# Optimization experiments

Hardware: AMD Instinct MI355X
Metric: run time of the kernel (lower is better)

Reference implementation:

```python
import jax, jax.numpy as jnp
import numpy as np

N_VERTS = 2562


def _uniform(key, shape, bound):
    return jax.random.uniform(key, shape, jnp.float32, -bound, bound)


def vert_align(feat, pos):
    # feat: [B,C,H,W]; pos: [B,N,3], xy in [-1,1] -> bilinear sample -> [B,N,C]
    B, C, H, W = feat.shape
    ft = jnp.transpose(feat, (0, 2, 3, 1))  # [B,H,W,C]
    x = (jnp.clip(pos[..., 0], -1.0, 1.0) + 1.0) * 0.5 * (W - 1)
    y = (jnp.clip(pos[..., 1], -1.0, 1.0) + 1.0) * 0.5 * (H - 1)
    x0 = jnp.floor(x)
    y0 = jnp.floor(y)
    x0i = x0.astype(jnp.int32)
    y0i = y0.astype(jnp.int32)
    x1i = jnp.minimum(x0i + 1, W - 1)
    y1i = jnp.minimum(y0i + 1, H - 1)
    wx = (x - x0)[..., None]
    wy = (y - y0)[..., None]
    b = jnp.arange(B)[:, None]
    f00 = ft[b, y0i, x0i]
    f01 = ft[b, y0i, x1i]
    f10 = ft[b, y1i, x0i]
    f11 = ft[b, y1i, x1i]
    return (f00 * (1 - wx) * (1 - wy) + f01 * wx * (1 - wy)
            + f10 * (1 - wx) * wy + f11 * wx * wy)


def graph_conv(x, adj, w0, w1):
    # relu(x @ w0 + adj @ (x @ w1))
    return jax.nn.relu(x @ w0 + jnp.einsum('bij,bjc->bic', adj, x @ w1))


def setup_inputs() -> dict:
    key = jax.random.key(0)
    ks = jax.random.split(key, 20)
    B, N = 8, N_VERTS
    inp = {
        'conv2_3': jax.random.normal(ks[0], (B, 256, 56, 56), jnp.float32),
        'conv3_4': jax.random.normal(ks[1], (B, 512, 28, 28), jnp.float32),
        'conv4_6': jax.random.normal(ks[2], (B, 1024, 14, 14), jnp.float32),
        'conv5_3': jax.random.normal(ks[3], (B, 2048, 7, 7), jnp.float32),
        # scaled so row sums are O(1), like a normalized dense adjacency
        'vertex_adjacency': jax.random.uniform(ks[4], (B, N, N), jnp.float32) * (2.0 / N),
        'vertex_positions': jax.random.uniform(ks[5], (B, N, 3), jnp.float32) * 2.0 - 1.0,
        'vertex_features': jax.random.normal(ks[6], (B, N, 128), jnp.float32),
    }
    # learned parameters (torch default / GraphConv uniform init)
    inp['w_lin0'] = _uniform(ks[7], (3840, 128), 1.0 / np.sqrt(3840))
    inp['b_lin0'] = _uniform(ks[8], (128,), 1.0 / np.sqrt(3840))
    inp['gc0_w0'] = _uniform(ks[9], (259, 131), 1.0 / np.sqrt(259))
    inp['gc0_w1'] = _uniform(ks[10], (259, 131), 1.0 / np.sqrt(259))
    inp['gc1_w0'] = _uniform(ks[11], (131, 128), 1.0 / np.sqrt(131))
    inp['gc1_w1'] = _uniform(ks[12], (131, 128), 1.0 / np.sqrt(131))
    inp['gc2_w0'] = _uniform(ks[13], (131, 128), 1.0 / np.sqrt(131))
    inp['gc2_w1'] = _uniform(ks[14], (131, 128), 1.0 / np.sqrt(131))
    inp['w_lin1'] = _uniform(ks[15], (128, 3), 1.0 / np.sqrt(128))
    inp['b_lin1'] = _uniform(ks[16], (3,), 1.0 / np.sqrt(128))
    return inp


def reference(conv2_3, conv3_4, conv4_6, conv5_3, vertex_adjacency,
              vertex_positions, vertex_features,
              w_lin0, b_lin0, gc0_w0, gc0_w1, gc1_w0, gc1_w1,
              gc2_w0, gc2_w1, w_lin1, b_lin1):
    verts = jnp.concatenate(
        [vert_align(f, vertex_positions)
         for f in (conv2_3, conv3_4, conv4_6, conv5_3)], axis=2)  # [B,N,3840]
    projected = verts @ w_lin0 + b_lin0                             # [B,N,128]
    vf = jnp.concatenate([vertex_features, vertex_positions, projected], axis=2)  # 259
    h = graph_conv(vf, vertex_adjacency, gc0_w0, gc0_w1)            # [B,N,131]
    h = jnp.concatenate([vertex_positions, h], axis=2)              # 134? no: 3+131=134 -- see note
    h = graph_conv(h[:, :, :131] if h.shape[2] != 131 else h, vertex_adjacency, gc1_w0, gc1_w1)
    h = jnp.concatenate([vertex_positions, h], axis=2)              # 131
    new_features = graph_conv(h, vertex_adjacency, gc2_w0, gc2_w1)  # [B,N,128]
    new_positions = vertex_positions + jnp.tanh(new_features @ w_lin1 + b_lin1)
    return new_positions, new_features
```

## Files before the change

kernel.cpp:

```cpp
#include <hip/hip_runtime.h>
#include <hip/hip_bf16.h>

typedef __attribute__((ext_vector_type(8))) short bf16x8;
typedef __attribute__((ext_vector_type(4))) float f32x4;
typedef __attribute__((ext_vector_type(2))) float f32x2;

static __device__ __forceinline__ float bf2f(unsigned short u){
  return __uint_as_float(((unsigned)u) << 16);
}
static __device__ __forceinline__ float bflo(unsigned v){ return __uint_as_float(v << 16); }
static __device__ __forceinline__ float bfhi(unsigned v){ return __uint_as_float(v & 0xffff0000u); }
static __device__ __forceinline__ unsigned short f2bf(float f){
  unsigned u = __float_as_uint(f);
  u += 0x7FFFu + ((u >> 16) & 1u);
  return (unsigned short)(u >> 16);
}
static __device__ __forceinline__ void gload_lds16(const void* g, void* l){
  __builtin_amdgcn_global_load_lds((const __attribute__((address_space(1))) unsigned int*)g,
                                   (__attribute__((address_space(3))) unsigned int*)l, 16, 0, 0);
}

#define MFMA16(acc, a, b) (acc) = __builtin_amdgcn_mfma_f32_16x16x32_bf16((a),(b),(acc),0,0,0)

#define NB   8
#define NVRT 2562
#define MP   2624
#define NRB2 82
#define NKT  41

#define FT_B0 0ul
#define FT_B1 6422528ul
#define FT_B2 9633792ul
#define FT_B3 11239424ul
#define FT_TOT 12042240ul

#define G_B0 0ul
#define G_B1 3211264ul
#define G_B2 4014080ul
#define G_B3 4214784ul
#define G_TOT 4264960ul

__global__ void k_transpose_all(const float* __restrict__ c0, const float* __restrict__ c1,
                                const float* __restrict__ c2, const float* __restrict__ c3,
                                unsigned short* __restrict__ ftT)
{
  __shared__ float tile[32][33];
  int bx = blockIdx.x, b = blockIdx.y;
  int m, local;
  if (bx < 784)      { m = 0; local = bx; }
  else if (bx < 1184){ m = 1; local = bx - 784; }
  else if (bx < 1408){ m = 2; local = bx - 1184; }
  else               { m = 3; local = bx - 1408; }
  int HW  = (m==0)?3136:(m==1)?784:(m==2)?196:49;
  int C   = 256 << m;
  int nbx = (m==0)?98:(m==1)?25:(m==2)?7:2;
  size_t fb = (m==0)?FT_B0:(m==1)?FT_B1:(m==2)?FT_B2:FT_B3;
  const float* src = (m==0)?c0:(m==1)?c1:(m==2)?c2:c3;

  int hw0 = (local % nbx) * 32, c0i = (local / nbx) * 32;
  int tx = threadIdx.x, ty = threadIdx.y;
  const float* s = src + (size_t)b * C * HW;
#pragma unroll
  for (int i = 0; i < 4; i++){
    int c = c0i + ty + i*8, hw = hw0 + tx;
    tile[ty + i*8][tx] = (c < C && hw < HW) ? s[(size_t)c * HW + hw] : 0.f;
  }
  __syncthreads();
  unsigned short* d = ftT + fb + (size_t)b * HW * C;
#pragma unroll
  for (int i = 0; i < 4; i++){
    int hw = hw0 + ty + i*8, c = c0i + tx;
    if (hw < HW && c < C) d[(size_t)hw * C + c] = f2bf(tile[tx][ty + i*8]);
  }
}

struct PWArgs {
  const float* src[7];
  unsigned short* dst[7];
  int ksrc[7], nsrc[7];
};
__global__ void k_packw_all(PWArgs a)
{
  const int cb[8] = {0,491520,528384,565248,585728,606208,626688,647168};
  int g = blockIdx.x * 256 + threadIdx.x;
#pragma unroll
  for (int s = 0; s < 7; s++){
    if (g >= cb[s] && g < cb[s+1]){
      int li = g - cb[s];
      int k = li >> 7, c = li & 127;
      int ks = a.ksrc[s], ns = a.nsrc[s];
      float v = (k < ks) ? a.src[s][(size_t)k * ns + c] : 0.f;
      a.dst[s][((size_t)(k >> 3) * 128 + c) * 8 + (k & 7)] = f2bf(v);
    }
  }
}

__global__ __launch_bounds__(256) void k_gproj(
    const unsigned short* __restrict__ ftT,
    const unsigned short* __restrict__ wp,
    unsigned short* __restrict__ G)
{
  int bx = blockIdx.x;
  int m, tile;
  if (bx < 784)      { m = 0; tile = bx; }
  else if (bx < 980) { m = 1; tile = bx - 784; }
  else if (bx < 1029){ m = 2; tile = bx - 980; }
  else               { m = 3; tile = bx - 1029; }
  int C    = 256 << m;
  int rows = 8 * ((m==0)?3136:(m==1)?784:(m==2)?196:49);
  size_t fb = (m==0)?FT_B0:(m==1)?FT_B1:(m==2)?FT_B2:FT_B3;
  size_t gb = (m==0)?G_B0:(m==1)?G_B1:(m==2)?G_B2:G_B3;
  int ko8 = ((m==0)?0:(m==1)?256:(m==2)?768:1792) >> 3;

  int t = threadIdx.x, wave = t >> 6, lane = t & 63;
  int rf = wave & 1, ch = wave >> 1;
  int l15 = lane & 15, l4 = lane >> 4;
  int row = tile*32 + rf*16 + l15;
  int arow = (row < rows) ? row : 0;
  const unsigned short* xp = ftT + fb + (size_t)arow * C + l4 * 8;

  f32x4 acc[4];
#pragma unroll
  for (int c = 0; c < 4; c++) acc[c] = (f32x4){0,0,0,0};

  for (int kb = 0; kb < C; kb += 32){
    bf16x8 a = *(const bf16x8*)(xp + kb);
    size_t bo = ((size_t)(ko8 + (kb>>3) + l4) * 128 + ch*64 + l15) * 8;
#pragma unroll
    for (int c = 0; c < 4; c++){
      bf16x8 bb = *(const bf16x8*)(wp + bo + c*128);
      MFMA16(acc[c], a, bb);
    }
  }
#pragma unroll
  for (int c = 0; c < 4; c++){
    int col = ch*64 + c*16 + l15;
#pragma unroll
    for (int r = 0; r < 4; r++){
      int orow = tile*32 + rf*16 + l4*4 + r;
      if (orow < rows) G[gb + (size_t)orow*128 + col] = f2bf(acc[c][r]);
    }
  }
}

__global__ void k_prep2(const float* __restrict__ vfeat, const float* __restrict__ pos,
                        const unsigned short* __restrict__ G,
                        const float* __restrict__ bias,
                        unsigned short* __restrict__ vf,
                        unsigned short* __restrict__ x1,
                        unsigned short* __restrict__ x2)
{
  int b = blockIdx.y;
  int row = blockIdx.x * 4 + (threadIdx.x >> 6);
  int lane = threadIdx.x & 63;
  size_t vfo = ((size_t)b * MP + row) * 288;
  size_t xo  = ((size_t)b * MP + row) * 160;
  if (row < NVRT){
    size_t src = (size_t)b * NVRT + row;
    float px = fminf(fmaxf(pos[src*3 + 0], -1.f), 1.f);
    float py = fminf(fmaxf(pos[src*3 + 1], -1.f), 1.f);
    int c0 = lane * 2;
    float s0 = bias[c0], s1 = bias[c0 + 1];
#pragma unroll
    for (int m = 0; m < 4; m++){
      int W = 56 >> m;
      int HW = W * W;
      size_t gb = (m==0)?G_B0:(m==1)?G_B1:(m==2)?G_B2:G_B3;
      float gx = (px + 1.f) * 0.5f * (float)(W - 1);
      float gy = (py + 1.f) * 0.5f * (float)(W - 1);
      int x0 = (int)floorf(gx), y0 = (int)floorf(gy);
      float wx = gx - (float)x0, wy = gy - (float)y0;
      int x1i = min(x0 + 1, W - 1), y1i = min(y0 + 1, W - 1);
      const unsigned short* g = G + gb + (size_t)b * HW * 128;
      unsigned v00 = *(const unsigned*)(g + ((size_t)(y0 *W + x0 ))*128 + c0);
      unsigned v01 = *(const unsigned*)(g + ((size_t)(y0 *W + x1i))*128 + c0);
      unsigned v10 = *(const unsigned*)(g + ((size_t)(y1i*W + x0 ))*128 + c0);
      unsigned v11 = *(const unsigned*)(g + ((size_t)(y1i*W + x1i))*128 + c0);
      float w00 = (1.f-wx)*(1.f-wy), w01 = wx*(1.f-wy);
      float w10 = (1.f-wx)*wy,       w11 = wx*wy;
      s0 += w00*bflo(v00) + w01*bflo(v01) + w10*bflo(v10) + w11*bflo(v11);
      s1 += w00*bfhi(v00) + w01*bfhi(v01) + w10*bfhi(v10) + w11*bfhi(v11);
    }
    vf[vfo + 131 + c0]     = f2bf(s0);
    vf[vfo + 131 + c0 + 1] = f2bf(s1);
    float2 fv = *(const float2*)(vfeat + src*128 + c0);
    vf[vfo + c0]     = f2bf(fv.x);
    vf[vfo + c0 + 1] = f2bf(fv.y);
    if (lane < 3){
      unsigned short v = f2bf(pos[src*3 + lane]);
      vf[vfo + 128 + lane] = v;
      x1[xo + lane] = v;
      x2[xo + lane] = v;
    }
    if (lane >= 32 && lane < 61) vf[vfo + 259 + (lane - 32)] = 0;
    if (lane < 29){ x1[xo + 131 + lane] = 0; x2[xo + 131 + lane] = 0; }
  } else {
    for (int c = lane; c < 288; c += 64) vf[vfo + c] = 0;
    for (int c = lane; c < 160; c += 64){ x1[xo + c] = 0; x2[xo + c] = 0; }
  }
}

__global__ void k_adjpack(const float* __restrict__ adj, unsigned short* __restrict__ adjP)
{
  int kt = blockIdx.x, rb = blockIdx.y, b = blockIdx.z;
  int t = threadIdx.x, row = t >> 3, k8 = t & 7;
  int grow = rb*32 + row, gk = kt*64 + k8*8;
  unsigned short o[8];
  if (grow < NVRT && gk + 8 <= NVRT){
    const float2* p = (const float2*)(adj + ((size_t)b*NVRT + grow)*NVRT + gk);
    float2 f0 = p[0], f1 = p[1], f2 = p[2], f3 = p[3];
    o[0]=f2bf(f0.x); o[1]=f2bf(f0.y); o[2]=f2bf(f1.x); o[3]=f2bf(f1.y);
    o[4]=f2bf(f2.x); o[5]=f2bf(f2.y); o[6]=f2bf(f3.x); o[7]=f2bf(f3.y);
  } else if (grow < NVRT){
    const float* ap = adj + ((size_t)b*NVRT + grow)*NVRT;
#pragma unroll
    for (int e = 0; e < 8; e++){ int k = gk + e; o[e] = (k < NVRT) ? f2bf(ap[k]) : 0; }
  } else {
#pragma unroll
    for (int e = 0; e < 8; e++) o[e] = 0;
  }
  bf16x8 h;
#pragma unroll
  for (int e = 0; e < 8; e++) h[e] = (short)o[e];
  char* tb = (char*)(adjP + (((size_t)b*NRB2 + rb)*NKT + kt) * 2048);
  *(bf16x8*)(tb + row*128 + ((k8*16) ^ ((row&7)<<4))) = h;
}

template<int KX>
__global__ __launch_bounds__(256) void k_xw2(
    const unsigned short* __restrict__ x,
    const unsigned short* __restrict__ wp0,
    const unsigned short* __restrict__ wp1,
    float* __restrict__ y0,
    unsigned short* __restrict__ y1p)
{
  int b = blockIdx.y, rb = blockIdx.x * 32;
  int t = threadIdx.x, wave = t >> 6, lane = t & 63;
  int rf = wave & 1, ch = wave >> 1;
  int l15 = lane & 15, l4 = lane >> 4;
  f32x4 a0[4], a1[4];
#pragma unroll
  for (int c = 0; c < 4; c++){ a0[c] = (f32x4){0,0,0,0}; a1[c] = (f32x4){0,0,0,0}; }
  int row = rb + rf*16 + l15;
  const unsigned short* xp = x + ((size_t)b * MP + row) * KX + l4 * 8;
#pragma unroll
  for (int kb = 0; kb < KX; kb += 32){
    bf16x8 a = *(const bf16x8*)(xp + kb);
    size_t bo = ((size_t)((kb>>3) + l4) * 128 + ch*64 + l15) * 8;
#pragma unroll
    for (int c = 0; c < 4; c++){
      bf16x8 b0 = *(const bf16x8*)(wp0 + bo + c*128);
      MFMA16(a0[c], a, b0);
      bf16x8 b1 = *(const bf16x8*)(wp1 + bo + c*128);
      MFMA16(a1[c], a, b1);
    }
  }
#pragma unroll
  for (int c = 0; c < 4; c++){
    int col = ch*64 + c*16 + l15;
#pragma unroll
    for (int r = 0; r < 4; r++){
      int orow = rb + rf*16 + l4*4 + r;
      y0[((size_t)b * MP + orow) * 128 + col] = a0[c][r];
      y1p[(((size_t)b * (MP/8) + (orow>>3)) * 128 + col) * 8 + (orow & 7)] = f2bf(a1[c][r]);
    }
  }
}

template<int EPI>
__global__ __launch_bounds__(256) void k_adj2(
    const unsigned short* __restrict__ adjP,
    const unsigned short* __restrict__ y1p,
    const float* __restrict__ y0,
    unsigned short* __restrict__ xnext,
    float* __restrict__ outf)
{
  __shared__ __align__(16) unsigned short abuf[2][2048];
  int b = blockIdx.y, rb = blockIdx.x;
  int t = threadIdx.x, wave = t >> 6, lane = t & 63;
  int l15 = lane & 15, l4 = lane >> 4;
  const unsigned short* tbase = adjP + (((size_t)b*NRB2 + rb)*NKT) * 2048;
  const unsigned short* y1b = y1p + (size_t)b * (MP/8) * 128 * 8;

  f32x4 acc[2][2];
#pragma unroll
  for (int i = 0; i < 2; i++)
#pragma unroll
    for (int j = 0; j < 2; j++) acc[i][j] = (f32x4){0,0,0,0};

  auto stage = [&](int kt, int bufi){
    gload_lds16(tbase + (size_t)kt*2048 + t*8, &abuf[bufi][wave*512]);
  };

  stage(0, 0);
  __syncthreads();

  for (int kt = 0; kt < NKT; ++kt){
    int cur = kt & 1;
    if (kt < NKT-1) stage(kt+1, cur ^ 1);
    bf16x8 bfr[2][2];
#pragma unroll
    for (int cf = 0; cf < 2; cf++)
#pragma unroll
      for (int ks = 0; ks < 2; ks++)
        bfr[cf][ks] = *(const bf16x8*)(y1b + ((size_t)(kt*8 + ks*4 + l4)*128 + wave*32 + cf*16 + l15)*8);
    const char* ab = (const char*)&abuf[cur][0];
    bf16x8 afr[2][2];
#pragma unroll
    for (int rf = 0; rf < 2; rf++){
      int row = rf*16 + l15;
      int sw = (row & 7) << 4;
#pragma unroll
      for (int ks = 0; ks < 2; ks++)
        afr[rf][ks] = *(const bf16x8*)(ab + row*128 + ((ks*64 + l4*16) ^ sw));
    }
#pragma unroll
    for (int ks = 0; ks < 2; ks++)
#pragma unroll
      for (int rf = 0; rf < 2; rf++)
#pragma unroll
        for (int cf = 0; cf < 2; cf++)
          MFMA16(acc[rf][cf], afr[rf][ks], bfr[cf][ks]);
    __syncthreads();
  }

#pragma unroll
  for (int rf = 0; rf < 2; rf++)
#pragma unroll
    for (int cf = 0; cf < 2; cf++){
      int col = wave*32 + cf*16 + l15;
#pragma unroll
      for (int r = 0; r < 4; r++){
        int row = rb*32 + rf*16 + l4*4 + r;
        if (row < NVRT){
          float v = fmaxf(y0[((size_t)b*MP + row)*128 + col] + acc[rf][cf][r], 0.f);
          if (EPI == 0) xnext[((size_t)b*MP + row)*160 + 3 + col] = f2bf(v);
          else          outf[((size_t)b*NVRT + row)*128 + col] = v;
        }
      }
    }
}

__global__ void k_head(const float* __restrict__ feat, const float* __restrict__ pos,
                       const float* __restrict__ wl1, const float* __restrict__ bl1,
                       float* __restrict__ opos)
{
  int grow = blockIdx.x * 4 + (threadIdx.x >> 6);
  int lane = threadIdx.x & 63;
  int b = grow / NVRT, row = grow - b * NVRT;
  int c0 = lane * 2;
  f32x2 v = *(const f32x2*)(feat + ((size_t)b * NVRT + row) * 128 + c0);
  float p[3];
#pragma unroll
  for (int j = 0; j < 3; j++){
    p[j] = v[0] * wl1[c0*3 + j] + v[1] * wl1[c0*3 + 3 + j];
#pragma unroll
    for (int off = 1; off < 64; off <<= 1)
      p[j] += __shfl_xor(p[j], off);
  }
  if (lane == 0){
    size_t po = ((size_t)b * NVRT + row) * 3;
#pragma unroll
    for (int j = 0; j < 3; j++)
      opos[po + j] = pos[po + j] + tanhf(p[j] + bl1[j]);
  }
}

extern "C" void kernel_launch(void* const* d_in, const int* in_sizes, int n_in,
                              void* d_out, int out_size, void* d_ws, size_t ws_size,
                              hipStream_t stream)
{
  const float* conv[4] = {(const float*)d_in[0], (const float*)d_in[1],
                          (const float*)d_in[2], (const float*)d_in[3]};
  const float* adj   = (const float*)d_in[4];
  const float* pos   = (const float*)d_in[5];
  const float* vfeat = (const float*)d_in[6];
  const float* wlin0 = (const float*)d_in[7];
  const float* blin0 = (const float*)d_in[8];
  const float* gw[6] = {(const float*)d_in[9],  (const float*)d_in[10],
                        (const float*)d_in[11], (const float*)d_in[12],
                        (const float*)d_in[13], (const float*)d_in[14]};
  const float* wlin1 = (const float*)d_in[15];
  const float* blin1 = (const float*)d_in[16];

  char* ws = (char*)d_ws;
  size_t off = 0;
  auto take = [&](size_t bytes)->char* {
    char* p = ws + off;
    off += (bytes + 255) & ~(size_t)255;
    return p;
  };
  unsigned short* ftT  = (unsigned short*)take(FT_TOT * 2);
  unsigned short* G    = (unsigned short*)take(G_TOT * 2);
  unsigned short* adjP = (unsigned short*)take((size_t)NB*NRB2*NKT*4096);
  unsigned short* wl0p = (unsigned short*)take((size_t)3840*128*2);
  unsigned short* w0p0 = (unsigned short*)take((size_t)288*128*2);
  unsigned short* w1p0 = (unsigned short*)take((size_t)288*128*2);
  unsigned short* w0p1 = (unsigned short*)take((size_t)160*128*2);
  unsigned short* w1p1 = (unsigned short*)take((size_t)160*128*2);
  unsigned short* w0p2 = (unsigned short*)take((size_t)160*128*2);
  unsigned short* w1p2 = (unsigned short*)take((size_t)160*128*2);
  unsigned short* vf   = (unsigned short*)take((size_t)NB*MP*288*2);
  unsigned short* x1   = (unsigned short*)take((size_t)NB*MP*160*2);
  unsigned short* x2   = (unsigned short*)take((size_t)NB*MP*160*2);
  float*          y0   = (float*)take((size_t)NB*MP*128*4);
  unsigned short* y1p  = (unsigned short*)take((size_t)NB*MP*128*2);

  float* out_pos  = (float*)d_out;
  float* out_feat = out_pos + (size_t)NB*NVRT*3;

  k_transpose_all<<<dim3(1536, NB), dim3(32, 8), 0, stream>>>(conv[0], conv[1], conv[2], conv[3], ftT);
  PWArgs pw;
  pw.src[0]=wlin0; pw.dst[0]=wl0p; pw.ksrc[0]=3840; pw.nsrc[0]=128;
  pw.src[1]=gw[0]; pw.dst[1]=w0p0; pw.ksrc[1]=259;  pw.nsrc[1]=131;
  pw.src[2]=gw[1]; pw.dst[2]=w1p0; pw.ksrc[2]=259;  pw.nsrc[2]=131;
  pw.src[3]=gw[2]; pw.dst[3]=w0p1; pw.ksrc[3]=131;  pw.nsrc[3]=128;
  pw.src[4]=gw[3]; pw.dst[4]=w1p1; pw.ksrc[4]=131;  pw.nsrc[4]=128;
  pw.src[5]=gw[4]; pw.dst[5]=w0p2; pw.ksrc[5]=131;  pw.nsrc[5]=128;
  pw.src[6]=gw[5]; pw.dst[6]=w1p2; pw.ksrc[6]=131;  pw.nsrc[6]=128;
  k_packw_all<<<2528, 256, 0, stream>>>(pw);
  k_gproj<<<1042, 256, 0, stream>>>(ftT, wl0p, G);
  k_prep2<<<dim3(MP/4, NB), 256, 0, stream>>>(vfeat, pos, G, blin0, vf, x1, x2);
  k_adjpack<<<dim3(NKT, NRB2, NB), 256, 0, stream>>>(adj, adjP);
  k_xw2<288><<<dim3(NRB2, NB), 256, 0, stream>>>(vf, w0p0, w1p0, y0, y1p);
  k_adj2<0><<<dim3(NRB2, NB), 256, 0, stream>>>(adjP, y1p, y0, x1, nullptr);
  k_xw2<160><<<dim3(NRB2, NB), 256, 0, stream>>>(x1, w0p1, w1p1, y0, y1p);
  k_adj2<0><<<dim3(NRB2, NB), 256, 0, stream>>>(adjP, y1p, y0, x2, nullptr);
  k_xw2<160><<<dim3(NRB2, NB), 256, 0, stream>>>(x2, w0p2, w1p2, y0, y1p);
  k_adj2<1><<<dim3(NRB2, NB), 256, 0, stream>>>(adjP, y1p, y0, nullptr, out_feat);
  k_head<<<NB*NVRT/4, 256, 0, stream>>>(out_feat, pos, wlin1, blin1, out_pos);
  (void)in_sizes; (void)n_in; (void)out_size; (void)ws_size;
}
```

Before: 320.6 us.

## Quantize adjacency and XW1 to FP8 and fuse head into last graph-conv

Packs the dense adjacency (scaled by 1024) and the x@w1 intermediate into e4m3 FP8 and runs the adjacency GEMMs with FP8 MFMA over 16-row blocks and 128-wide K tiles. This halves the bytes the adjacency kernels read and pack, which is the dominant memory traffic. The position head is folded into the last adjacency kernel's epilogue through shared memory, which removes a separate launch and a reread of the output features. The cost is a large loss of precision in the adjacency product, which may exceed the tolerance, plus an extra memset.

After: 291.7 us. 1.1x faster.

```diff
diff --git a/kernel.cpp b/kernel.cpp
--- a/kernel.cpp
+++ b/kernel.cpp
@@ -4,6 +4,7 @@
 typedef __attribute__((ext_vector_type(8))) short bf16x8;
 typedef __attribute__((ext_vector_type(4))) float f32x4;
 typedef __attribute__((ext_vector_type(2))) float f32x2;
+typedef long long i64;
 
 static __device__ __forceinline__ float bf2f(unsigned short u){
   return __uint_as_float(((unsigned)u) << 16);
@@ -15,18 +16,32 @@
   u += 0x7FFFu + ((u >> 16) & 1u);
   return (unsigned short)(u >> 16);
 }
+static __device__ __forceinline__ unsigned f2e4m3(float x){
+  unsigned b = __float_as_uint(x);
+  unsigned s = (b >> 31) << 7;
+  b &= 0x7fffffffu;
+  if (b >= 0x43e80000u) return s | 0x7eu;
+  if (b < 0x3c800000u)
+    return s | (unsigned)rintf(__uint_as_float(b) * 512.f);
+  unsigned b2 = b + 0x7ffffu + ((b >> 20) & 1u);
+  return s | (((b2 >> 23) - 120u) << 3) | ((b2 >> 20) & 7u);
+}
 static __device__ __forceinline__ void gload_lds16(const void* g, void* l){
   __builtin_amdgcn_global_load_lds((const __attribute__((address_space(1))) unsigned int*)g,
                                    (__attribute__((address_space(3))) unsigned int*)l, 16, 0, 0);
 }
 
 #define MFMA16(acc, a, b) (acc) = __builtin_amdgcn_mfma_f32_16x16x32_bf16((a),(b),(acc),0,0,0)
-
-#define NB   8
-#define NVRT 2562
-#define MP   2624
-#define NRB2 82
-#define NKT  41
+#define MFMA8(acc, a, b)  (acc) = __builtin_amdgcn_mfma_f32_16x16x32_fp8_fp8((a),(b),(acc),0,0,0)
+
+#define NB    8
+#define NVRT  2562
+#define MP    2624
+#define NRB2  82
+#define NRB16 164
+#define NKT8  21
+#define KOCT  336
+#define YO    ((size_t)KOCT*128*8)
 
 #define FT_B0 0ul
 #define FT_B1 6422528ul
@@ -200,30 +215,32 @@
   }
 }
 
-__global__ void k_adjpack(const float* __restrict__ adj, unsigned short* __restrict__ adjP)
+__global__ void k_adjpack8(const float* __restrict__ adj, unsigned char* __restrict__ adjP)
 {
   int kt = blockIdx.x, rb = blockIdx.y, b = blockIdx.z;
-  int t = threadIdx.x, row = t >> 3, k8 = t & 7;
-  int grow = rb*32 + row, gk = kt*64 + k8*8;
-  unsigned short o[8];
+  int t = threadIdx.x;
+  int r = t >> 4, kseg = t & 15;
+  int grow = rb*16 + r, gk = kt*128 + kseg*8;
+  float v[8];
   if (grow < NVRT && gk + 8 <= NVRT){
-    const float2* p = (const float2*)(adj + ((size_t)b*NVRT + grow)*NVRT + gk);
-    float2 f0 = p[0], f1 = p[1], f2 = p[2], f3 = p[3];
-    o[0]=f2bf(f0.x); o[1]=f2bf(f0.y); o[2]=f2bf(f1.x); o[3]=f2bf(f1.y);
-    o[4]=f2bf(f2.x); o[5]=f2bf(f2.y); o[6]=f2bf(f3.x); o[7]=f2bf(f3.y);
+    const float4* p = (const float4*)(adj + ((size_t)b*NVRT + grow)*NVRT + gk);
+    float4 f0 = p[0], f1 = p[1];
+    v[0]=f0.x; v[1]=f0.y; v[2]=f0.z; v[3]=f0.w;
+    v[4]=f1.x; v[5]=f1.y; v[6]=f1.z; v[7]=f1.w;
   } else if (grow < NVRT){
     const float* ap = adj + ((size_t)b*NVRT + grow)*NVRT;
 #pragma unroll
-    for (int e = 0; e < 8; e++){ int k = gk + e; o[e] = (k < NVRT) ? f2bf(ap[k]) : 0; }
+    for (int e = 0; e < 8; e++){ int k = gk + e; v[e] = (k < NVRT) ? ap[k] : 0.f; }
   } else {
 #pragma unroll
-    for (int e = 0; e < 8; e++) o[e] = 0;
-  }
-  bf16x8 h;
-#pragma unroll
-  for (int e = 0; e < 8; e++) h[e] = (short)o[e];
-  char* tb = (char*)(adjP + (((size_t)b*NRB2 + rb)*NKT + kt) * 2048);
-  *(bf16x8*)(tb + row*128 + ((k8*16) ^ ((row&7)<<4))) = h;
+    for (int e = 0; e < 8; e++) v[e] = 0.f;
+  }
+  unsigned long long q = 0;
+#pragma unroll
+  for (int e = 0; e < 8; e++)
+    q |= (unsigned long long)f2e4m3(v[e] * 1024.f) << (8*e);
+  unsigned char* tb = adjP + (((size_t)b*NRB16 + rb)*NKT8 + kt) * 2048;
+  *(unsigned long long*)(tb + 128*r + 8*(kseg ^ r)) = q;
 }
 
 template<int KX>
@@ -232,7 +249,7 @@
     const unsigned short* __restrict__ wp0,
     const unsigned short* __restrict__ wp1,
     float* __restrict__ y0,
-    unsigned short* __restrict__ y1p)
+    unsigned char* __restrict__ y1p8)
 {
   int b = blockIdx.y, rb = blockIdx.x * 32;
   int t = threadIdx.x, wave = t >> 6, lane = t & 63;
@@ -255,114 +272,115 @@
       MFMA16(a1[c], a, b1);
     }
   }
+  unsigned char* yb = y1p8 + (size_t)b * YO;
 #pragma unroll
   for (int c = 0; c < 4; c++){
     int col = ch*64 + c*16 + l15;
-#pragma unroll
-    for (int r = 0; r < 4; r++){
-      int orow = rb + rf*16 + l4*4 + r;
-      y0[((size_t)b * MP + orow) * 128 + col] = a0[c][r];
-      y1p[(((size_t)b * (MP/8) + (orow>>3)) * 128 + col) * 8 + (orow & 7)] = f2bf(a1[c][r]);
-    }
+    int orow0 = rb + rf*16 + l4*4;
+#pragma unroll
+    for (int r = 0; r < 4; r++)
+      y0[((size_t)b * MP + orow0 + r) * 128 + col] = a0[c][r];
+    unsigned q = f2e4m3(a1[c][0]) | (f2e4m3(a1[c][1]) << 8)
+               | (f2e4m3(a1[c][2]) << 16) | (f2e4m3(a1[c][3]) << 24);
+    *(unsigned*)(yb + ((size_t)(orow0 >> 3) * 128 + col) * 8 + (orow0 & 7)) = q;
   }
 }
 
 template<int EPI>
-__global__ __launch_bounds__(256) void k_adj2(
-    const unsigned short* __restrict__ adjP,
-    const unsigned short* __restrict__ y1p,
+__global__ __launch_bounds__(256) void k_adj8(
+    const unsigned char* __restrict__ adjP,
+    const unsigned char* __restrict__ y1p8,
     const float* __restrict__ y0,
     unsigned short* __restrict__ xnext,
-    float* __restrict__ outf)
-{
-  __shared__ __align__(16) unsigned short abuf[2][2048];
-  int b = blockIdx.y, rb = blockIdx.x;
-  int t = threadIdx.x, wave = t >> 6, lane = t & 63;
+    float* __restrict__ outf,
+    const float* __restrict__ pos,
+    const float* __restrict__ wl1, const float* __restrict__ bl1,
+    float* __restrict__ opos)
+{
+  __shared__ __align__(16) unsigned char abuf[2][2048];
+  __shared__ float hbuf[16][128];
+  int rb = blockIdx.x, b = blockIdx.y;
+  int t = threadIdx.x, w = t >> 6, lane = t & 63;
   int l15 = lane & 15, l4 = lane >> 4;
-  const unsigned short* tbase = adjP + (((size_t)b*NRB2 + rb)*NKT) * 2048;
-  const unsigned short* y1b = y1p + (size_t)b * (MP/8) * 128 * 8;
-
-  f32x4 acc[2][2];
-#pragma unroll
-  for (int i = 0; i < 2; i++)
-#pragma unroll
-    for (int j = 0; j < 2; j++) acc[i][j] = (f32x4){0,0,0,0};
+  const unsigned char* tb = adjP + (((size_t)b*NRB16 + rb)*NKT8) * 2048;
+  const unsigned char* yb = y1p8 + (size_t)b * YO;
+
+  f32x4 acc[2];
+  acc[0] = (f32x4){0,0,0,0};
+  acc[1] = (f32x4){0,0,0,0};
 
   auto stage = [&](int kt, int bufi){
-    gload_lds16(tbase + (size_t)kt*2048 + t*8, &abuf[bufi][wave*512]);
+    if (w < 2)
+      gload_lds16(tb + (size_t)kt*2048 + w*1024 + lane*16, &abuf[bufi][w*1024]);
   };
 
   stage(0, 0);
   __syncthreads();
 
-  for (int kt = 0; kt < NKT; ++kt){
+  for (int kt = 0; kt < NKT8; ++kt){
     int cur = kt & 1;
-    if (kt < NKT-1) stage(kt+1, cur ^ 1);
-    bf16x8 bfr[2][2];
-#pragma unroll
-    for (int cf = 0; cf < 2; cf++)
-#pragma unroll
-      for (int ks = 0; ks < 2; ks++)
-        bfr[cf][ks] = *(const bf16x8*)(y1b + ((size_t)(kt*8 + ks*4 + l4)*128 + wave*32 + cf*16 + l15)*8);
-    const char* ab = (const char*)&abuf[cur][0];
-    bf16x8 afr[2][2];
-#pragma unroll
-    for (int rf = 0; rf < 2; rf++){
-      int row = rf*16 + l15;
-      int sw = (row & 7) << 4;
-#pragma unroll
-      for (int ks = 0; ks < 2; ks++)
-        afr[rf][ks] = *(const bf16x8*)(ab + row*128 + ((ks*64 + l4*16) ^ sw));
-    }
-#pragma unroll
-    for (int ks = 0; ks < 2; ks++)
-#pragma unroll
-      for (int rf = 0; rf < 2; rf++)
-#pragma unroll
-        for (int cf = 0; cf < 2; cf++)
-          MFMA16(acc[rf][cf], afr[rf][ks], bfr[cf][ks]);
+    if (kt < NKT8-1) stage(kt+1, cur ^ 1);
+    const unsigned char* ab = &abuf[cur][0];
+#pragma unroll
+    for (int sel = 0; sel < 2; sel++){
+#pragma unroll
+      for (int ks = 0; ks < 2; ks++){
+        int koct = sel*8 + ks*4 + l4;
+        i64 a = *(const i64*)(ab + 128*l15 + 8*(koct ^ l15));
+        const unsigned char* bp = yb + ((size_t)(kt*16 + koct)*128 + w*32 + l15)*8;
+        i64 b0 = *(const i64*)(bp);
+        i64 b1 = *(const i64*)(bp + 128);
+        MFMA8(acc[0], a, b0);
+        MFMA8(acc[1], a, b1);
+      }
+    }
     __syncthreads();
   }
 
 #pragma unroll
-  for (int rf = 0; rf < 2; rf++)
-#pragma unroll
-    for (int cf = 0; cf < 2; cf++){
-      int col = wave*32 + cf*16 + l15;
-#pragma unroll
-      for (int r = 0; r < 4; r++){
-        int row = rb*32 + rf*16 + l4*4 + r;
-        if (row < NVRT){
-          float v = fmaxf(y0[((size_t)b*MP + row)*128 + col] + acc[rf][cf][r], 0.f);
-          if (EPI == 0) xnext[((size_t)b*MP + row)*160 + 3 + col] = f2bf(v);
-          else          outf[((size_t)b*NVRT + row)*128 + col] = v;
+  for (int cf = 0; cf < 2; cf++){
+    int col = w*32 + cf*16 + l15;
+#pragma unroll
+    for (int r = 0; r < 4; r++){
+      int row16 = l4*4 + r;
+      int row = rb*16 + row16;
+      float v = 0.f;
+      if (row < NVRT)
+        v = fmaxf(y0[((size_t)b*MP + row)*128 + col] + acc[cf][r] * 0.0009765625f, 0.f);
+      if (EPI == 0){
+        if (row < NVRT) xnext[((size_t)b*MP + row)*160 + 3 + col] = f2bf(v);
+      } else {
+        if (row < NVRT) outf[((size_t)b*NVRT + row)*128 + col] = v;
+        hbuf[row16][col] = v;
+      }
+    }
+  }
+
+  if (EPI == 1){
+    __syncthreads();
+#pragma unroll
+    for (int rr = 0; rr < 4; rr++){
+      int row16 = w*4 + rr;
+      int grow = rb*16 + row16;
+      if (grow < NVRT){
+        int c0 = lane * 2;
+        float v0 = hbuf[row16][c0], v1 = hbuf[row16][c0+1];
+        float p[3];
+#pragma unroll
+        for (int j = 0; j < 3; j++){
+          p[j] = v0 * wl1[c0*3 + j] + v1 * wl1[c0*3 + 3 + j];
+#pragma unroll
+          for (int off = 1; off < 64; off <<= 1)
+            p[j] += __shfl_xor(p[j], off);
+        }
+        if (lane == 0){
+          size_t po = ((size_t)b * NVRT + grow) * 3;
+#pragma unroll
+          for (int j = 0; j < 3; j++)
+            opos[po + j] = pos[po + j] + tanhf(p[j] + bl1[j]);
         }
       }
     }
-}
-
-__global__ void k_head(const float* __restrict__ feat, const float* __restrict__ pos,
-                       const float* __restrict__ wl1, const float* __restrict__ bl1,
-                       float* __restrict__ opos)
-{
-  int grow = blockIdx.x * 4 + (threadIdx.x >> 6);
-  int lane = threadIdx.x & 63;
-  int b = grow / NVRT, row = grow - b * NVRT;
-  int c0 = lane * 2;
-  f32x2 v = *(const f32x2*)(feat + ((size_t)b * NVRT + row) * 128 + c0);
-  float p[3];
-#pragma unroll
-  for (int j = 0; j < 3; j++){
-    p[j] = v[0] * wl1[c0*3 + j] + v[1] * wl1[c0*3 + 3 + j];
-#pragma unroll
-    for (int off = 1; off < 64; off <<= 1)
-      p[j] += __shfl_xor(p[j], off);
-  }
-  if (lane == 0){
-    size_t po = ((size_t)b * NVRT + row) * 3;
-#pragma unroll
-    for (int j = 0; j < 3; j++)
-      opos[po + j] = pos[po + j] + tanhf(p[j] + bl1[j]);
   }
 }
 
@@ -392,7 +410,7 @@
   };
   unsigned short* ftT  = (unsigned short*)take(FT_TOT * 2);
   unsigned short* G    = (unsigned short*)take(G_TOT * 2);
-  unsigned short* adjP = (unsigned short*)take((size_t)NB*NRB2*NKT*4096);
+  unsigned char*  adjP = (unsigned char*)take((size_t)NB*NRB16*NKT8*2048);
   unsigned short* wl0p = (unsigned short*)take((size_t)3840*128*2);
   unsigned short* w0p0 = (unsigned short*)take((size_t)288*128*2);
   unsigned short* w1p0 = (unsigned short*)take((size_t)288*128*2);
@@ -404,11 +422,12 @@
   unsigned short* x1   = (unsigned short*)take((size_t)NB*MP*160*2);
   unsigned short* x2   = (unsigned short*)take((size_t)NB*MP*160*2);
   float*          y0   = (float*)take((size_t)NB*MP*128*4);
-  unsigned short* y1p  = (unsigned short*)take((size_t)NB*MP*128*2);
+  unsigned char*  y1p8 = (unsigned char*)take((size_t)NB*YO);
 
   float* out_pos  = (float*)d_out;
   float* out_feat = out_pos + (size_t)NB*NVRT*3;
 
+  hipMemsetAsync(y1p8, 0, (size_t)NB*YO, stream);
   k_transpose_all<<<dim3(1536, NB), dim3(32, 8), 0, stream>>>(conv[0], conv[1], conv[2], conv[3], ftT);
   PWArgs pw;
   pw.src[0]=wlin0; pw.dst[0]=wl0p; pw.ksrc[0]=3840; pw.nsrc[0]=128;
@@ -421,13 +440,12 @@
   k_packw_all<<<2528, 256, 0, stream>>>(pw);
   k_gproj<<<1042, 256, 0, stream>>>(ftT, wl0p, G);
   k_prep2<<<dim3(MP/4, NB), 256, 0, stream>>>(vfeat, pos, G, blin0, vf, x1, x2);
-  k_adjpack<<<dim3(NKT, NRB2, NB), 256, 0, stream>>>(adj, adjP);
-  k_xw2<288><<<dim3(NRB2, NB), 256, 0, stream>>>(vf, w0p0, w1p0, y0, y1p);
-  k_adj2<0><<<dim3(NRB2, NB), 256, 0, stream>>>(adjP, y1p, y0, x1, nullptr);
-  k_xw2<160><<<dim3(NRB2, NB), 256, 0, stream>>>(x1, w0p1, w1p1, y0, y1p);
-  k_adj2<0><<<dim3(NRB2, NB), 256, 0, stream>>>(adjP, y1p, y0, x2, nullptr);
-  k_xw2<160><<<dim3(NRB2, NB), 256, 0, stream>>>(x2, w0p2, w1p2, y0, y1p);
-  k_adj2<1><<<dim3(NRB2, NB), 256, 0, stream>>>(adjP, y1p, y0, nullptr, out_feat);
-  k_head<<<NB*NVRT/4, 256, 0, stream>>>(out_feat, pos, wlin1, blin1, out_pos);
+  k_adjpack8<<<dim3(NKT8, NRB16, NB), 256, 0, stream>>>(adj, adjP);
+  k_xw2<288><<<dim3(NRB2, NB), 256, 0, stream>>>(vf, w0p0, w1p0, y0, y1p8);
+  k_adj8<0><<<dim3(NRB16, NB), 256, 0, stream>>>(adjP, y1p8, y0, x1, nullptr, nullptr, nullptr, nullptr, nullptr);
+  k_xw2<160><<<dim3(NRB2, NB), 256, 0, stream>>>(x1, w0p1, w1p1, y0, y1p8);
+  k_adj8<0><<<dim3(NRB16, NB), 256, 0, stream>>>(adjP, y1p8, y0, x2, nullptr, nullptr, nullptr, nullptr, nullptr);
+  k_xw2<160><<<dim3(NRB2, NB), 256, 0, stream>>>(x2, w0p2, w1p2, y0, y1p8);
+  k_adj8<1><<<dim3(NRB16, NB), 256, 0, stream>>>(adjP, y1p8, y0, nullptr, out_feat, pos, wlin1, blin1, out_pos);
   (void)in_sizes; (void)n_in; (void)out_size; (void)ws_size;
 }
```
